# Performance work log

Hardware: AMD Instinct MI355X
Metric: run time of the kernel (lower is better)

## Reference

```python
import jax, jax.numpy as jnp
import numpy as np

EPS = 1e-3  # matches torch module eps
NUM_FEATURES = 64


def setup_inputs() -> dict:
    key = jax.random.key(0)
    X = jax.random.normal(key, (128, NUM_FEATURES, 56, 56), dtype=jnp.float32)
    return {"X": X}


def reference(X):
    # Training-mode decorrelated batch norm (ZCA whitening via eigendecomposition).
    N, C = X.shape[0], X.shape[1]
    # [N, C, H, W] -> [C, N*H*W]
    x = jnp.reshape(jnp.swapaxes(X, 0, 1), (C, -1))
    m = x.shape[1]
    mean = jnp.mean(x, axis=-1, keepdims=True)
    xc = x - mean
    # sigma = eps*I + (1/m) * xc @ xc^T   (C x C, SPD)
    sigma = EPS * jnp.eye(C, dtype=X.dtype) + (xc @ xc.T) / m
    # SVD of an SPD matrix == eigendecomposition; use symmetric eigh.
    eig, u = jnp.linalg.eigh(sigma)
    # wm = u @ diag(eig^-1/2) @ u^T  (inverse matrix square root)
    wm = (u * jax.lax.rsqrt(eig)) @ u.T
    xn = wm @ xc  # whiten
    # [C, N*H*W] -> [N, C, H, W]
    Xn = jnp.swapaxes(jnp.reshape(xn, (C, N) + X.shape[2:]), 0, 1)
    return Xn
```

## Files before the change

### kernel.cpp

```cpp
#include <hip/hip_runtime.h>
#include <stdint.h>

#define CCH   64
#define HWSZ  3136
#define NB    128
#define MCOLS 401408
#define TK    128
#define NTILES 3136
#define LDK   136
#define LDB   72
#define SLOT  4160
#define WS_TAIL 12416
#define RG    32
#define K1MAX 1024

typedef short bf16x8 __attribute__((ext_vector_type(8)));
typedef float f32x4  __attribute__((ext_vector_type(4)));

__device__ __forceinline__ unsigned short f2bf(float f) {
    union { float f; uint32_t u; } v; v.f = f;
    uint32_t r = v.u + 0x7fffu + ((v.u >> 16) & 1u);
    return (unsigned short)(r >> 16);
}
__device__ __forceinline__ float bf2f(unsigned short h) {
    union { uint32_t u; float f; } v; v.u = ((uint32_t)h) << 16; return v.f;
}

__global__ __launch_bounds__(256) void k1_gram(const float* __restrict__ X,
                                               float* __restrict__ part,
                                               int nb) {
    __shared__ __align__(16) unsigned short tile[CCH * LDK];
    const int tid = threadIdx.x;
    const int w = tid >> 6, l = tid & 63;

    f32x4 acc[4];
    #pragma unroll
    for (int b = 0; b < 4; ++b) acc[b] = (f32x4){0.f, 0.f, 0.f, 0.f};
    float sacc[16];
    #pragma unroll
    for (int i = 0; i < 16; ++i) sacc[i] = 0.f;

    float2 xv[16];

    uint32_t t = blockIdx.x;
    {
        const uint32_t s = t * TK + 2u * (uint32_t)l;
        const uint32_t n = s / HWSZ;
        const uint32_t hw = s - n * HWSZ;
        const size_t base = (size_t)n * (CCH * HWSZ) + hw + (size_t)w * HWSZ;
        #pragma unroll
        for (int i = 0; i < 16; ++i)
            xv[i] = *(const float2*)(X + base + (size_t)i * (4u * HWSZ));
    }

    for (;;) {
        __syncthreads();
        #pragma unroll
        for (int i = 0; i < 16; ++i) {
            sacc[i] += xv[i].x + xv[i].y;
            const int c = 4 * i + w;
            *(uint32_t*)&tile[c * LDK + 2 * l] =
                (uint32_t)f2bf(xv[i].x) | ((uint32_t)f2bf(xv[i].y) << 16);
        }
        __syncthreads();

        const uint32_t tn = t + (uint32_t)nb;
        const bool more = tn < NTILES;
        if (more) {
            const uint32_t s = tn * TK + 2u * (uint32_t)l;
            const uint32_t n = s / HWSZ;
            const uint32_t hw = s - n * HWSZ;
            const size_t base = (size_t)n * (CCH * HWSZ) + hw + (size_t)w * HWSZ;
            #pragma unroll
            for (int i = 0; i < 16; ++i)
                xv[i] = *(const float2*)(X + base + (size_t)i * (4u * HWSZ));
        }

        #pragma unroll
        for (int k0 = 0; k0 < TK; k0 += 32) {
            const int koff = k0 + ((l >> 4) << 3);
            const bf16x8 fa = *(const bf16x8*)&tile[(16 * w + (l & 15)) * LDK + koff];
            #pragma unroll
            for (int bj = 0; bj < 4; ++bj) {
                const bf16x8 fb = *(const bf16x8*)&tile[(16 * bj + (l & 15)) * LDK + koff];
                acc[bj] = __builtin_amdgcn_mfma_f32_16x16x32_bf16(fa, fb, acc[bj], 0, 0, 0);
            }
        }

        if (!more) break;
        t = tn;
    }

    float* pg = part + (size_t)blockIdx.x * SLOT;
    #pragma unroll
    for (int bj = 0; bj < 4; ++bj) {
        #pragma unroll
        for (int r = 0; r < 4; ++r) {
            const int row = 16 * w + ((l >> 4) << 2) + r;
            const int col = 16 * bj + (l & 15);
            pg[row * 64 + col] = acc[bj][r];
        }
    }
    #pragma unroll
    for (int i = 0; i < 16; ++i) {
        float v = sacc[i];
        #pragma unroll
        for (int m = 32; m > 0; m >>= 1) v += __shfl_xor(v, m, 64);
        if (l == 0) pg[4096 + 4 * i + w] = v;
    }
}

__global__ __launch_bounds__(256) void k1b1_reduce(const float* __restrict__ part,
                                                   float* __restrict__ part2,
                                                   int nb) {
    const int bx = blockIdx.x;
    const int g = bx / 17;
    const int e = (bx - g * 17) * 256 + threadIdx.x;
    if (e >= SLOT) return;
    float a0 = 0.f, a1 = 0.f, a2 = 0.f, a3 = 0.f;
    int b = g;
    for (; b + 3 * RG < nb; b += 4 * RG) {
        a0 += part[(size_t)b * SLOT + e];
        a1 += part[(size_t)(b + RG) * SLOT + e];
        a2 += part[(size_t)(b + 2 * RG) * SLOT + e];
        a3 += part[(size_t)(b + 3 * RG) * SLOT + e];
    }
    for (; b < nb; b += RG) a0 += part[(size_t)b * SLOT + e];
    part2[(size_t)g * SLOT + e] = (a0 + a1) + (a2 + a3);
}

__global__ __launch_bounds__(256) void k1b2_reduce(const float* __restrict__ part2,
                                                   float* __restrict__ out) {
    const int e = blockIdx.x * 256 + threadIdx.x;
    if (e >= SLOT) return;
    float a0 = 0.f, a1 = 0.f, a2 = 0.f, a3 = 0.f;
    #pragma unroll
    for (int b = 0; b < RG; b += 4) {
        a0 += part2[(size_t)b * SLOT + e];
        a1 += part2[(size_t)(b + 1) * SLOT + e];
        a2 += part2[(size_t)(b + 2) * SLOT + e];
        a3 += part2[(size_t)(b + 3) * SLOT + e];
    }
    out[e] = (a0 + a1) + (a2 + a3);
}

__device__ __forceinline__ bf16x8 ldfrag_h(const unsigned short* H, int rowbase, int k0, int l) {
    const int row = rowbase + (l & 15);
    const int koff = k0 + ((l >> 4) << 3);
    return *(const bf16x8*)&H[row * LDB + koff];
}
__device__ __forceinline__ bf16x8 ldfrag_lo(const float* F, bf16x8 hi, int rowbase, int k0, int l) {
    const int row = rowbase + (l & 15);
    const int koff = k0 + ((l >> 4) << 3);
    const float* p = F + row * 64 + koff;
    bf16x8 lo;
    #pragma unroll
    for (int j = 0; j < 8; ++j)
        lo[j] = (short)f2bf(p[j] - bf2f((unsigned short)hi[j]));
    return lo;
}

__device__ void mm_plain(const unsigned short* Lh, const unsigned short* Rh,
                         unsigned short* DH, float* DF, int tid) {
    const int w = tid >> 6, l = tid & 63;
    f32x4 acc[4];
    #pragma unroll
    for (int b = 0; b < 4; ++b) acc[b] = (f32x4){0.f, 0.f, 0.f, 0.f};
    #pragma unroll
    for (int k0 = 0; k0 < 64; k0 += 32) {
        const bf16x8 la = ldfrag_h(Lh, 16 * w, k0, l);
        #pragma unroll
        for (int b = 0; b < 4; ++b) {
            const bf16x8 rb = ldfrag_h(Rh, 16 * b, k0, l);
            acc[b] = __builtin_amdgcn_mfma_f32_16x16x32_bf16(la, rb, acc[b], 0, 0, 0);
        }
    }
    __syncthreads();
    #pragma unroll
    for (int b = 0; b < 4; ++b) {
        #pragma unroll
        for (int r = 0; r < 4; ++r) {
            const int row = 16 * w + ((l >> 4) << 2) + r;
            const int col = 16 * b + (l & 15);
            const float v = acc[b][r];
            if (DH) DH[row * LDB + col] = f2bf(v);
            if (DF) DF[row * 64 + col] = v;
        }
    }
    __syncthreads();
}

__device__ void mm_split(const unsigned short* Lh, const float* Lf,
                         const unsigned short* Rh, const float* Rf,
                         unsigned short* DH, float* DF, int tid) {
    const int w = tid >> 6, l = tid & 63;
    f32x4 acc[4];
    #pragma unroll
    for (int b = 0; b < 4; ++b) acc[b] = (f32x4){0.f, 0.f, 0.f, 0.f};
    #pragma unroll
    for (int k0 = 0; k0 < 64; k0 += 32) {
        const bf16x8 lah = ldfrag_h(Lh, 16 * w, k0, l);
        const bf16x8 lal = ldfrag_lo(Lf, lah, 16 * w, k0, l);
        #pragma unroll
        for (int b = 0; b < 4; ++b) {
            const bf16x8 rbh = ldfrag_h(Rh, 16 * b, k0, l);
            const bf16x8 rbl = ldfrag_lo(Rf, rbh, 16 * b, k0, l);
            acc[b] = __builtin_amdgcn_mfma_f32_16x16x32_bf16(lah, rbh, acc[b], 0, 0, 0);
            acc[b] = __builtin_amdgcn_mfma_f32_16x16x32_bf16(lah, rbl, acc[b], 0, 0, 0);
            acc[b] = __builtin_amdgcn_mfma_f32_16x16x32_bf16(lal, rbh, acc[b], 0, 0, 0);
        }
    }
    __syncthreads();
    #pragma unroll
    for (int b = 0; b < 4; ++b) {
        #pragma unroll
        for (int r = 0; r < 4; ++r) {
            const int row = 16 * w + ((l >> 4) << 2) + r;
            const int col = 16 * b + (l & 15);
            const float v = acc[b][r];
            if (DH) DH[row * LDB + col] = f2bf(v);
            if (DF) DF[row * 64 + col] = v;
        }
    }
    __syncthreads();
}

__global__ __launch_bounds__(256) void k2_ns(float* __restrict__ ws) {
    const float* gram = ws;
    const float* sums = ws + 4096;
    float* wm = ws + 4160;
    float* bvec = ws + 8256;
    float* Ag = ws + 8320;

    __shared__ float Zf[4096];
    __shared__ float Sf[4096];
    __shared__ __align__(16) unsigned short Ah[64 * LDB];
    __shared__ __align__(16) unsigned short ZhA[64 * LDB];
    __shared__ __align__(16) unsigned short Bh[64 * LDB];
    __shared__ float mu[64];
    __shared__ float sred[1];

    const int tid = threadIdx.x;
    const float invm = 1.0f / (float)MCOLS;

    if (tid < 64) mu[tid] = sums[tid] * invm;
    __syncthreads();

    #pragma unroll
    for (int j = 0; j < 16; ++j) {
        const int e = tid * 16 + j;
        const int i = e >> 6, c = e & 63;
        Sf[e] = gram[e] * invm - mu[i] * mu[c] + ((i == c) ? 1e-3f : 0.0f);
    }
    __syncthreads();

    if (tid < 64) {
        float rs = 0.f;
        #pragma unroll
        for (int j = 0; j < 64; ++j) {
            const int c = (j + tid) & 63;
            rs += fabsf(Sf[tid * 64 + c]);
        }
        #pragma unroll
        for (int m = 32; m > 0; m >>= 1) rs = fmaxf(rs, __shfl_xor(rs, m, 64));
        if (tid == 0) sred[0] = rs;
    }
    __syncthreads();
    const float s = sred[0];
    const float invs = 1.0f / s;

    #pragma unroll
    for (int j = 0; j < 16; ++j) {
        const int e = tid * 16 + j;
        const int i = e >> 6, c = e & 63;
        const float a = Sf[e] * invs;
        Ag[e] = a;
        Ah[i * LDB + c] = f2bf(a);
        const float z = (i == c) ? 1.0f : 0.0f;
        Zf[e] = z;
        ZhA[i * LDB + c] = f2bf(z);
    }
    __syncthreads();

    for (int itn = 0; itn < 4; ++itn) {
        mm_plain(ZhA, ZhA, Bh, nullptr, tid);
        mm_plain(Ah, Bh, Bh, nullptr, tid);
        mm_plain(ZhA, Bh, nullptr, Sf, tid);
        #pragma unroll
        for (int j = 0; j < 16; ++j) {
            const int e = tid * 16 + j;
            const int i = e >> 6, c = e & 63;
            const float z = 1.5f * Zf[e] - 0.5f * Sf[e];
            Zf[e] = z;
            ZhA[i * LDB + c] = f2bf(z);
        }
        __syncthreads();
    }

    mm_split(ZhA, Zf, ZhA, Zf, Bh, Sf, tid);
    mm_split(Ah, Ag, Bh, Sf, Bh, Sf, tid);
    mm_split(ZhA, Zf, Bh, Sf, nullptr, Sf, tid);

    const float wsq = 1.0f / sqrtf(s);
    #pragma unroll
    for (int j = 0; j < 16; ++j) {
        const int e = tid * 16 + j;
        const float z = 1.5f * Zf[e] - 0.5f * Sf[e];
        Zf[e] = z;
        wm[e] = z * wsq;
    }
    __syncthreads();

    if (tid < 64) {
        float acc = 0.f;
        #pragma unroll
        for (int j = 0; j < 64; ++j) {
            const int c = (j + tid) & 63;
            acc += Zf[tid * 64 + c] * mu[c];
        }
        bvec[tid] = acc * wsq;
    }
}

__global__ __launch_bounds__(256) void k3_whiten(const float* __restrict__ X,
                                                 const float* __restrict__ wm,
                                                 const float* __restrict__ bvec,
                                                 float* __restrict__ out) {
    const int tid = threadIdx.x;
    const int w = tid >> 6, l = tid & 63;
    const uint32_t chunk = blockIdx.x * 4u + (uint32_t)w;
    const uint32_t n = chunk / 49u;
    const uint32_t hw = (chunk - n * 49u) * 64u + (uint32_t)l;
    const size_t base = (size_t)n * (CCH * HWSZ) + hw;

    float acc[64];
    #pragma unroll
    for (int c = 0; c < 64; ++c) acc[c] = 0.f;

    float xv = X[base];
    for (int cp = 0; cp < 64; ++cp) {
        const float xn = (cp < 63) ? X[base + (size_t)(cp + 1) * HWSZ] : 0.f;
        const float* wr = wm + cp * 64;
        #pragma unroll
        for (int c = 0; c < 64; ++c) acc[c] = fmaf(wr[c], xv, acc[c]);
        xv = xn;
    }
    #pragma unroll
    for (int c = 0; c < 64; ++c)
        out[base + (size_t)c * HWSZ] = acc[c] - bvec[c];
}

extern "C" void kernel_launch(void* const* d_in, const int* in_sizes, int n_in,
                              void* d_out, int out_size, void* d_ws, size_t ws_size,
                              hipStream_t stream) {
    (void)in_sizes; (void)n_in; (void)out_size;
    const float* X = (const float*)d_in[0];
    float* out = (float*)d_out;
    float* ws = (float*)d_ws;

    long avail = (long)(ws_size / sizeof(float)) - WS_TAIL - (long)RG * SLOT;
    int nb = (int)(avail / SLOT);
    if (nb > K1MAX) nb = K1MAX;
    if (nb < 1) nb = 1;

    float* part = ws + WS_TAIL;
    float* part2 = part + (size_t)nb * SLOT;

    k1_gram<<<nb, 256, 0, stream>>>(X, part, nb);
    k1b1_reduce<<<17 * RG, 256, 0, stream>>>(part, part2, nb);
    k1b2_reduce<<<17, 256, 0, stream>>>(part2, ws);
    k2_ns<<<1, 256, 0, stream>>>(ws);
    k3_whiten<<<1568, 256, 0, stream>>>(X, ws + 4160, ws + 8256, out);
}
```

Baseline: 269.6 us.

## Stage X tile in LDS and split output channels across waves in whiten

The whitening kernel now has each block cooperatively load a 64-channel by 64-pixel tile of X into shared memory with vector loads. Each of the four waves then computes 16 output channels for the same 64 pixels instead of one wave computing all 64 channels. This cuts per-thread accumulator registers from 64 to 16, which should raise occupancy, and it quadruples the grid size. The cost is an LDS round trip and a barrier per block, and X is read from global memory only once per block.

New measurement: 251.1 us. 6.9% less time.

```diff
diff --git a/kernel.cpp b/kernel.cpp
--- a/kernel.cpp
+++ b/kernel.cpp
@@ -326,28 +326,40 @@
                                                  const float* __restrict__ wm,
                                                  const float* __restrict__ bvec,
                                                  float* __restrict__ out) {
+    __shared__ float xs[64 * 64];
     const int tid = threadIdx.x;
-    const int w = tid >> 6, l = tid & 63;
-    const uint32_t chunk = blockIdx.x * 4u + (uint32_t)w;
-    const uint32_t n = chunk / 49u;
-    const uint32_t hw = (chunk - n * 49u) * 64u + (uint32_t)l;
-    const size_t base = (size_t)n * (CCH * HWSZ) + hw;
-
-    float acc[64];
-    #pragma unroll
-    for (int c = 0; c < 64; ++c) acc[c] = 0.f;
-
-    float xv = X[base];
+    const int l = tid & 63;
+    const int wq = __builtin_amdgcn_readfirstlane(tid >> 6) * 16;
+
+    const uint32_t g = blockIdx.x;
+    const uint32_t n = g / 49u;
+    const uint32_t hw0 = (g - n * 49u) * 64u;
+    const size_t base = (size_t)n * (CCH * HWSZ) + hw0;
+
+    #pragma unroll
+    for (int cb = 0; cb < 4; ++cb) {
+        const int cp = cb * 16 + (tid >> 4);
+        const int p4 = (tid & 15) * 4;
+        *(f32x4*)&xs[cp * 64 + p4] =
+            *(const f32x4*)(X + base + (size_t)cp * HWSZ + p4);
+    }
+    __syncthreads();
+
+    float acc[16];
+    #pragma unroll
+    for (int j = 0; j < 16; ++j) acc[j] = 0.f;
+
+    #pragma unroll 2
     for (int cp = 0; cp < 64; ++cp) {
-        const float xn = (cp < 63) ? X[base + (size_t)(cp + 1) * HWSZ] : 0.f;
-        const float* wr = wm + cp * 64;
-        #pragma unroll
-        for (int c = 0; c < 64; ++c) acc[c] = fmaf(wr[c], xv, acc[c]);
-        xv = xn;
-    }
-    #pragma unroll
-    for (int c = 0; c < 64; ++c)
-        out[base + (size_t)c * HWSZ] = acc[c] - bvec[c];
+        const float xv = xs[cp * 64 + l];
+        const float* wr = wm + cp * 64 + wq;
+        #pragma unroll
+        for (int j = 0; j < 16; ++j) acc[j] = fmaf(wr[j], xv, acc[j]);
+    }
+
+    #pragma unroll
+    for (int j = 0; j < 16; ++j)
+        out[base + (size_t)(wq + j) * HWSZ + l] = acc[j] - bvec[wq + j];
 }
 
 extern "C" void kernel_launch(void* const* d_in, const int* in_sizes, int n_in,
@@ -370,5 +382,5 @@
     k1b1_reduce<<<17 * RG, 256, 0, stream>>>(part, part2, nb);
     k1b2_reduce<<<17, 256, 0, stream>>>(part2, ws);
     k2_ns<<<1, 256, 0, stream>>>(ws);
-    k3_whiten<<<1568, 256, 0, stream>>>(X, ws + 4160, ws + 8256, out);
-}
+    k3_whiten<<<MCOLS / 64, 256, 0, stream>>>(X, ws + 4160, ws + 8256, out);
+}
```
